# Kernel tuning notes

Measured on AMD Instinct MI355X. Metric: run time of the kernel, lower is better.

## Reference

```python
import jax, jax.numpy as jnp
import numpy as np

N, T, D, H, E, ED = 4096, 16, 5, 128, 32768, 32

def _leaky(x):
    return jnp.where(x >= 0, x, 0.2 * x)

def _lstm(x, Wih, Whh, bih, bhh):
    # x: [N, T, D] -> hidden sequence [N, T, H]; PyTorch gate order i,f,g,o
    pre = jnp.einsum('ntd,gd->tng', x, Wih) + bih + bhh  # [T, N, 4H]
    Hd = Whh.shape[1]
    def step(carry, p):
        h, c = carry
        g = p + h @ Whh.T
        i, f, gg, o = jnp.split(g, 4, axis=-1)
        c = jax.nn.sigmoid(f) * c + jax.nn.sigmoid(i) * jnp.tanh(gg)
        h = jax.nn.sigmoid(o) * jnp.tanh(c)
        return (h, c), h
    z = jnp.zeros((x.shape[0], Hd), x.dtype)
    _, hs = jax.lax.scan(step, (z, z), pre)
    return jnp.swapaxes(hs, 0, 1)

def _sire(x, src, dst, efeat, Wq, bq, Wk, bk, We, be, Wr, br):
    # SIREConv with agg_type='sum': m = LeakyReLU(eq[dst]+ek[src]+e); sum over in-edges; then linear_relation
    eq = x @ Wq.T + bq            # [N, T, H]
    ek = x @ Wk.T + bk            # [N, T, H]
    e = efeat @ We.T + be         # [E, H]
    m = _leaky(eq[dst] + ek[src] + e[:, None, :])  # [E, T, H]
    ft = jax.ops.segment_sum(m, dst, num_segments=x.shape[0])  # [N, T, H]
    return ft @ Wr.T + br

def _forward(stock_features, srcs, dsts, efeats, sire_ps, lstm_p, attn_p, mlp_p):
    sf = stock_features / jnp.mean(stock_features, axis=1, keepdims=True)
    sr = _lstm(sf, *lstm_p)  # [N, T, H]
    outs = [sr]
    for s, d, ef, p in zip(srcs, dsts, efeats, sire_ps):
        outs.append(_sire(sr, s, d, ef, *p))
    cat = jnp.concatenate(outs, axis=-1)  # [N, T, 4H]
    aw = jax.nn.softmax(cat @ attn_p[0].T + attn_p[1], axis=-2)  # softmax over time
    pooled = jnp.sum(cat * aw, axis=-2)   # [N, 4H]
    W1, b1, W2, b2 = mlp_p
    h = _leaky(pooled @ W1.T + b1)
    out = _leaky(h @ W2.T + b2)           # [N, 1]
    return out / sf[:, -1, 0:1] - 1.0


def setup_inputs() -> dict:
    key = jax.random.key(0)
    ks = iter(jax.random.split(key, 64))
    def nrm(shape, s=0.05):
        return jax.random.normal(next(ks), shape, jnp.float32) * s
    inp = {}
    inp['stock_features'] = jax.random.uniform(next(ks), (N, T, D), jnp.float32) + 0.5
    for g in ['wiki', 'industry', 'corr']:
        inp[g + '_src'] = jax.random.randint(next(ks), (E,), 0, N, jnp.int32)
        inp[g + '_dst'] = jax.random.randint(next(ks), (E,), 0, N, jnp.int32)
        inp[g + '_efeat'] = nrm((E, ED), 1.0)
        inp[g + '_Wq'] = nrm((H, H)); inp[g + '_bq'] = nrm((H,))
        inp[g + '_Wk'] = nrm((H, H)); inp[g + '_bk'] = nrm((H,))
        inp[g + '_We'] = nrm((H, ED)); inp[g + '_be'] = nrm((H,))
        inp[g + '_Wr'] = nrm((H, H)); inp[g + '_br'] = nrm((H,))
    inp['lstm_Wih'] = nrm((4 * H, D)); inp['lstm_Whh'] = nrm((4 * H, H))
    inp['lstm_bih'] = nrm((4 * H,)); inp['lstm_bhh'] = nrm((4 * H,))
    inp['attn_W'] = nrm((1, 4 * H)); inp['attn_b'] = nrm((1,))
    inp['mlp_W1'] = nrm((H, 4 * H)); inp['mlp_b1'] = nrm((H,))
    inp['mlp_W2'] = nrm((1, H)); inp['mlp_b2'] = nrm((1,))
    return inp


def reference(stock_features, wiki_src, wiki_dst, wiki_efeat,
              wiki_Wq, wiki_bq, wiki_Wk, wiki_bk, wiki_We, wiki_be, wiki_Wr, wiki_br,
              industry_src, industry_dst, industry_efeat,
              industry_Wq, industry_bq, industry_Wk, industry_bk, industry_We, industry_be, industry_Wr, industry_br,
              corr_src, corr_dst, corr_efeat,
              corr_Wq, corr_bq, corr_Wk, corr_bk, corr_We, corr_be, corr_Wr, corr_br,
              lstm_Wih, lstm_Whh, lstm_bih, lstm_bhh,
              attn_W, attn_b, mlp_W1, mlp_b1, mlp_W2, mlp_b2):
    srcs = (wiki_src, industry_src, corr_src)
    dsts = (wiki_dst, industry_dst, corr_dst)
    efeats = (wiki_efeat, industry_efeat, corr_efeat)
    sire_ps = ((wiki_Wq, wiki_bq, wiki_Wk, wiki_bk, wiki_We, wiki_be, wiki_Wr, wiki_br),
               (industry_Wq, industry_bq, industry_Wk, industry_bk, industry_We, industry_be, industry_Wr, industry_br),
               (corr_Wq, corr_bq, corr_Wk, corr_bk, corr_We, corr_be, corr_Wr, corr_br))
    return _forward(stock_features, srcs, dsts, efeats, sire_ps,
                    (lstm_Wih, lstm_Whh, lstm_bih, lstm_bhh),
                    (attn_W, attn_b), (mlp_W1, mlp_b1, mlp_W2, mlp_b2))
```

## Files before the change

kernel.cpp:

```cpp
#include <hip/hip_runtime.h>
#include <cstdint>
#include <cstddef>

#define NS 4096
#define TS 16
#define DF 5
#define HD 128
#define EE 32768
#define EDD 32

typedef _Float16 h16;
typedef __attribute__((ext_vector_type(8))) _Float16 f16x8;
typedef __attribute__((ext_vector_type(2))) __fp16 fp16x2_n;
typedef __attribute__((ext_vector_type(4))) float f32x4;

__device__ __forceinline__ float sigmoidf_(float x){ return 1.f/(1.f+__expf(-x)); }
__device__ __forceinline__ float tanhf_(float x){ return 1.f - 2.f/(1.f+__expf(2.f*x)); }
__device__ __forceinline__ float leaky_(float x){ return x >= 0.f ? x : 0.2f*x; }

__device__ __forceinline__ unsigned pkh(float a, float b){
  union { fp16x2_n h; unsigned u; } x;
  x.h = __builtin_amdgcn_cvt_pkrtz(a, b);
  return x.u;
}
__device__ __forceinline__ void unpkh(unsigned u, float& a, float& b){
  union { unsigned u; fp16x2_n h; } x; x.u = u;
  a = (float)x.h.x; b = (float)x.h.y;
}
__device__ __forceinline__ f16x8 ld_h8(const h16* p){
  union { uint4 u; f16x8 v; } x; x.u = *(const uint4*)p; return x.v;
}

template<int AH, int CH>
__device__ __forceinline__ void gemm_dev(const void* Av, int lda,
    const float* __restrict__ Bp, int ldb, const float* __restrict__ bp,
    void* Cv, int ldc, int K, int act, size_t m0,
    h16* Asb, h16* Bsb)
{
  int tid = threadIdx.x;
  int wv = tid>>6, lane = tid&63, lm = lane&15, lq = lane>>4;
  f32x4 acc[2][8];
  #pragma unroll
  for (int mt=0;mt<2;mt++)
    #pragma unroll
    for (int nt=0;nt<8;nt++)
      acc[mt][nt] = (f32x4){0.f,0.f,0.f,0.f};

  for (int k0=0; k0<K; k0+=32){
    if (AH){
      const h16* A = (const h16*)Av;
      #pragma unroll
      for (int rep=0;rep<2;rep++){
        int idx = tid + rep*256;
        int row = idx>>2, c8 = idx&3;
        *(uint4*)&Asb[row*40 + c8*8] = *(const uint4*)&A[(m0+row)*(size_t)lda + k0 + c8*8];
      }
    } else {
      const float* A = (const float*)Av;
      #pragma unroll
      for (int rep=0;rep<4;rep++){
        int idx = tid + rep*256;
        int row = idx>>3, c4 = idx&7;
        float4 a = *(const float4*)&A[(m0+row)*(size_t)lda + k0 + c4*4];
        *(uint2*)&Asb[row*40 + c4*4] = make_uint2(pkh(a.x,a.y), pkh(a.z,a.w));
      }
    }
    #pragma unroll
    for (int rep=0;rep<4;rep++){
      int idx = tid + rep*256;
      int row = idx>>3, c4 = idx&7;
      float4 b = *(const float4*)&Bp[(size_t)row*ldb + k0 + c4*4];
      *(uint2*)&Bsb[row*40 + c4*4] = make_uint2(pkh(b.x,b.y), pkh(b.z,b.w));
    }
    __syncthreads();
    f16x8 afr[2], bfr[8];
    #pragma unroll
    for (int mt=0;mt<2;mt++)
      afr[mt] = ld_h8(&Asb[(wv*32 + mt*16 + lm)*40 + lq*8]);
    #pragma unroll
    for (int nt=0;nt<8;nt++)
      bfr[nt] = ld_h8(&Bsb[(nt*16 + lm)*40 + lq*8]);
    #pragma unroll
    for (int mt=0;mt<2;mt++)
      #pragma unroll
      for (int nt=0;nt<8;nt++)
        acc[mt][nt] = __builtin_amdgcn_mfma_f32_16x16x32_f16(afr[mt], bfr[nt], acc[mt][nt], 0,0,0);
    __syncthreads();
  }

  #pragma unroll
  for (int mt=0;mt<2;mt++){
    #pragma unroll
    for (int nt=0;nt<8;nt++){
      int col = nt*16 + lm;
      float bv = bp[col];
      #pragma unroll
      for (int i=0;i<4;i++){
        float o = acc[mt][nt][i] + bv;
        if (act) o = leaky_(o);
        size_t ridx = (m0 + wv*32 + mt*16 + lq*4 + i)*(size_t)ldc + col;
        if (CH) ((h16*)Cv)[ridx] = (h16)o;
        else    ((float*)Cv)[ridx] = o;
      }
    }
  }
}

__device__ void lstm8_dev(int blk, const float* __restrict__ sf,
                          const h16* __restrict__ WhhH,
                          const float* __restrict__ Wih, const float* __restrict__ bih,
                          const float* __restrict__ bhh, h16* __restrict__ cat,
                          char* smem)
{
  float* gates = (float*)smem;
  h16* hbuf = (h16*)(smem+16512);
  float* sfb = (float*)(smem+16512+2176);
  int tid = threadIdx.x;
  int n0 = blk*8;
  int wv = tid>>6, lane = tid&63, lm = lane&15, lq = lane>>4;

  f16x8 bfr[8][4];
  #pragma unroll
  for (int nt=0;nt<8;nt++){
    int g = wv*128 + nt*16 + lm;
    #pragma unroll
    for (int kt=0;kt<4;kt++)
      bfr[nt][kt] = *(const f16x8*)&WhhH[g*128 + kt*32 + lq*8];
  }

  int j = tid & 127;
  int rb = tid >> 7;
  float wih[4][5]; float bsum[4];
  #pragma unroll
  for (int gi=0; gi<4; gi++){
    int gc = gi*128 + j;
    #pragma unroll
    for (int d=0; d<5; d++) wih[gi][d] = Wih[gc*5+d];
    bsum[gi] = bih[gc] + bhh[gc];
  }
  float cst[4] = {0.f,0.f,0.f,0.f};

  for (int i=tid;i<544;i+=256) ((unsigned*)hbuf)[i] = 0;
  for (int i=tid;i<640;i+=256) sfb[i] = sf[(size_t)n0*80 + i];
  __syncthreads();

  f16x8 zf = {0,0,0,0,0,0,0,0};
  for (int t=0;t<16;t++){
    f16x8 af[4];
    #pragma unroll
    for (int kt=0;kt<4;kt++)
      af[kt] = (lm < 8) ? *(const f16x8*)&hbuf[lm*136 + kt*32 + lq*8] : zf;
    #pragma unroll
    for (int nt=0;nt<8;nt++){
      f32x4 acc = {0.f,0.f,0.f,0.f};
      #pragma unroll
      for (int kt=0;kt<4;kt++)
        acc = __builtin_amdgcn_mfma_f32_16x16x32_f16(af[kt], bfr[nt][kt], acc, 0,0,0);
      if (lq < 2){
        int col = wv*128 + nt*16 + lm;
        #pragma unroll
        for (int i=0;i<4;i++)
          gates[(lq*4+i)*516 + col] = acc[i];
      }
    }
    __syncthreads();
    #pragma unroll
    for (int q=0;q<4;q++){
      int r = rb + 2*q;
      const float* s = &sfb[r*80 + t*5];
      float pre[4];
      #pragma unroll
      for (int gi=0;gi<4;gi++){
        float a = bsum[gi];
        #pragma unroll
        for (int d=0;d<5;d++) a = fmaf(s[d], wih[gi][d], a);
        pre[gi] = a + gates[r*516 + gi*128 + j];
      }
      float iv = sigmoidf_(pre[0]);
      float fv = sigmoidf_(pre[1]);
      float gv = tanhf_(pre[2]);
      float ov = sigmoidf_(pre[3]);
      float c = fv*cst[q] + iv*gv;
      cst[q] = c;
      float h = ov*tanhf_(c);
      h16 hh = (h16)h;
      hbuf[r*136 + j] = hh;
      cat[(size_t)((n0+r)*16 + t)*512 + j] = hh;
    }
    __syncthreads();
  }
}

struct PP { const float* Wr[3]; };
__global__ __launch_bounds__(256)
void k_prolog(const float* __restrict__ x, float* __restrict__ sf,
              const float* __restrict__ Whh, h16* __restrict__ whhH,
              int* __restrict__ cnt, PP wr, h16* __restrict__ wrH)
{
  int b = blockIdx.x, tid = threadIdx.x;
  if (b < 48){
    int i = b*256 + tid;
    if (i < 3*4096) cnt[i] = 0;
  } else if (b < 128){
    int id = (b-48)*256 + tid;
    if (id < NS*DF){
      int n = id / DF, d = id % DF;
      const float* xp = x + (size_t)n*TS*DF + d;
      float s = 0.f;
      #pragma unroll
      for (int t=0;t<TS;t++) s += xp[t*DF];
      float inv = (float)TS / s;
      float* sp = sf + (size_t)n*TS*DF + d;
      #pragma unroll
      for (int t=0;t<TS;t++) sp[t*DF] = xp[t*DF]*inv;
    }
  } else if (b < 384){
    int i = (b-128)*256 + tid;
    whhH[i] = (h16)Whh[i];
  } else {
    int i = (b-384)*256 + tid;
    int g = i >> 14, r = i & 16383;
    wrH[i] = (h16)wr.Wr[g][r];
  }
}

struct M1 {
  const float *sf, *Wih, *bih, *bhh;
  const h16* WhhH;
  h16* cat;
  const float *ef[3]; const float *We[3]; const float *be[3];
  h16* eeb;
  const int* dst[3]; const int* src[3];
  int* cnt;
  int2* eidx2;
};
__global__ __launch_bounds__(256,2)
void k_mega1(M1 p)
{
  __shared__ __align__(16) char smem[21504];
  int b = blockIdx.x;
  if (b < 512){
    lstm8_dev(b, p.sf, p.WhhH, p.Wih, p.bih, p.bhh, p.cat, smem);
  } else if (b < 1280){
    int idx = b - 512;
    int proj = idx % 3, mt = idx / 3;
    h16* Asb = (h16*)smem;
    h16* Bsb = Asb + 128*40;
    gemm_dev<0,1>(p.ef[proj], 32, p.We[proj], 32, p.be[proj],
                  p.eeb + (size_t)proj*EE*128, 128, 32, 0, (size_t)mt*128, Asb, Bsb);
  } else {
    int idx = b - 1280;
    int g = idx >> 7, blk = idx & 127;
    int e = blk*256 + threadIdx.x;
    int d = p.dst[g][e];
    int s = p.src[g][e];
    int pos = atomicAdd(&p.cnt[g*4096 + d], 1);
    if (pos < 32) p.eidx2[((size_t)(g*4096 + d))*32 + pos] = make_int2(e, s);
  }
}

struct M2 {
  const h16* cat;
  const float* W[6]; const float* bias[6];
  h16* eqk;
};
__global__ __launch_bounds__(256)
void k_mega2(M2 p)
{
  __shared__ __align__(16) h16 Asb[128*40];
  __shared__ __align__(16) h16 Bsb[128*40];
  int b = blockIdx.x;
  int proj = b % 6, mt = b / 6;
  gemm_dev<1,1>(p.cat, 512, p.W[proj], 128, p.bias[proj],
                p.eqk + (size_t)proj*NS*TS*128, 128, 128, 0, (size_t)mt*128, Asb, Bsb);
}

struct EWP { const float* br[3]; };
__global__ __launch_bounds__(256)
void k_edgewr(const h16* __restrict__ eqk, const h16* __restrict__ eeb,
              const int* __restrict__ cnt, const int2* __restrict__ eidx2,
              const h16* __restrict__ wrH, EWP wp, h16* __restrict__ cat)
{
  __shared__ __align__(16) h16 ftS[16*136];
  int n = blockIdx.x;
  int g = blockIdx.y;
  const h16* eqb = eqk + (size_t)(2*g)  *NS*TS*128;
  const h16* ekb = eqk + (size_t)(2*g+1)*NS*TS*128;
  const h16* eeg = eeb + (size_t)g*EE*128;
  int tid = threadIdx.x;
  int wv = tid>>6, lane = tid&63, lm = lane&15, lq = lane>>4;

  const h16* wrg = wrH + (size_t)g*128*128;
  f16x8 bfr[2][4];
  #pragma unroll
  for (int nn=0;nn<2;nn++){
    int row = (wv*2+nn)*16 + lm;
    #pragma unroll
    for (int kt=0;kt<4;kt++)
      bfr[nn][kt] = ld_h8(&wrg[row*128 + kt*32 + lq*8]);
  }

  int t = tid>>4, hb = (tid&15)*8;
  size_t own = ((size_t)(n*16+t))*128 + hb;
  f16x8 eqv = ld_h8(&eqb[own]);
  const f16x8 c02 = {(h16)0.2f,(h16)0.2f,(h16)0.2f,(h16)0.2f,
                     (h16)0.2f,(h16)0.2f,(h16)0.2f,(h16)0.2f};
  float acc[8];
  #pragma unroll
  for (int j=0;j<8;j++) acc[j]=0.f;
  int ne = cnt[g*4096 + n]; if (ne > 32) ne = 32;
  const int2* el = eidx2 + ((size_t)(g*4096 + n))*32;
  for (int i=0;i<ne;i++){
    int2 es = el[i];
    f16x8 kv = ld_h8(&ekb[((size_t)(es.y*16+t))*128 + hb]);
    f16x8 ev = ld_h8(&eeg[(size_t)es.x*128 + hb]);
    f16x8 x = eqv + kv + ev;
    f16x8 lk = __builtin_elementwise_max(x, x*c02);
    #pragma unroll
    for (int j=0;j<8;j++) acc[j] += (float)lk[j];
  }
  uint4 o;
  o.x = pkh(acc[0],acc[1]); o.y = pkh(acc[2],acc[3]);
  o.z = pkh(acc[4],acc[5]); o.w = pkh(acc[6],acc[7]);
  *(uint4*)&ftS[t*136 + hb] = o;
  __syncthreads();

  f16x8 af[4];
  #pragma unroll
  for (int kt=0;kt<4;kt++)
    af[kt] = ld_h8(&ftS[lm*136 + kt*32 + lq*8]);
  const float* br = wp.br[g];
  h16* catp = cat + (size_t)(1+g)*128;
  #pragma unroll
  for (int nn=0; nn<2; nn++){
    int nt = wv*2 + nn;
    f32x4 a2 = {0.f,0.f,0.f,0.f};
    #pragma unroll
    for (int kt=0;kt<4;kt++)
      a2 = __builtin_amdgcn_mfma_f32_16x16x32_f16(af[kt], bfr[nn][kt], a2, 0,0,0);
    int colg = nt*16 + lm;
    float bv = br[colg];
    #pragma unroll
    for (int i=0;i<4;i++){
      int row = lq*4 + i;
      catp[((size_t)(n*16+row))*512 + colg] = (h16)(a2[i] + bv);
    }
  }
}

__global__ __launch_bounds__(256)
void k_attn(const h16* __restrict__ cat, const float* __restrict__ attnW,
            const float* __restrict__ attnB, h16* __restrict__ pooled)
{
  __shared__ h16 ct[16*512];
  __shared__ float sred[4][16];
  int n = blockIdx.x, tid = threadIdx.x;
  {
    const uint4* srcp = (const uint4*)(cat + (size_t)n*8192);
    uint4* dstp = (uint4*)ct;
    for (int i=tid;i<1024;i+=256) dstp[i] = srcp[i];
  }
  __syncthreads();
  int c0 = tid*2;
  float w0 = attnW[c0], w1 = attnW[c0+1];
  const unsigned* ctu = (const unsigned*)ct;
  float loc[16];
  #pragma unroll
  for (int t=0;t<16;t++){
    float a,b; unpkh(ctu[t*256 + tid], a, b);
    loc[t] = a*w0 + b*w1;
  }
  #pragma unroll
  for (int t=0;t<16;t++){
    float v = loc[t];
    for (int off=1; off<64; off<<=1) v += __shfl_xor(v, off, 64);
    loc[t]=v;
  }
  int wave = tid >> 6, lane = tid & 63;
  if (lane==0){
    #pragma unroll
    for (int t=0;t<16;t++) sred[wave][t]=loc[t];
  }
  __syncthreads();
  float s[16]; float m=-1e30f;
  float ab = attnB[0];
  #pragma unroll
  for (int t=0;t<16;t++){ s[t] = sred[0][t]+sred[1][t]+sred[2][t]+sred[3][t] + ab; m = fmaxf(m, s[t]); }
  float sum=0.f;
  #pragma unroll
  for (int t=0;t<16;t++){ s[t] = __expf(s[t]-m); sum += s[t]; }
  float inv = 1.f/sum;
  float p0=0.f,p1=0.f;
  #pragma unroll
  for (int t=0;t<16;t++){
    float a = s[t]*inv;
    float x,y; unpkh(ctu[t*256 + tid], x, y);
    p0 = fmaf(x, a, p0); p1 = fmaf(y, a, p1);
  }
  ((unsigned*)pooled)[(size_t)n*256 + tid] = pkh(p0,p1);
}

__global__ __launch_bounds__(256)
void k_mlp(const h16* __restrict__ pooled, const float* __restrict__ W1,
           const float* __restrict__ b1, h16* __restrict__ hmlp,
           const float* __restrict__ W2, const float* __restrict__ b2,
           const float* __restrict__ sf, float* __restrict__ out)
{
  __shared__ __align__(16) h16 Asb[128*40];
  __shared__ __align__(16) h16 Bsb[128*40];
  size_t m0 = (size_t)blockIdx.x*128;
  gemm_dev<1,1>(pooled, 512, W1, 512, b1, hmlp, 128, 512, 1, m0, Asb, Bsb);
  __syncthreads();
  int tid = threadIdx.x;
  int r = tid >> 1, o64 = (tid & 1)*64;
  const h16* hp = hmlp + (m0 + r)*128 + o64;
  float acc = 0.f;
  #pragma unroll
  for (int c=0; c<64; c++) acc = fmaf((float)hp[c], W2[o64 + c], acc);
  acc += __shfl_xor(acc, 1, 64);
  if ((tid & 1) == 0){
    float o = leaky_(acc + b2[0]);
    size_t n = m0 + r;
    out[n] = o / sf[n*80 + 75] - 1.f;
  }
}

extern "C" void kernel_launch(void* const* d_in, const int* in_sizes, int n_in,
                              void* d_out, int out_size, void* d_ws, size_t ws_size,
                              hipStream_t stream)
{
  const float* x    = (const float*)d_in[0];
  const float* Wih  = (const float*)d_in[34];
  const float* Whh  = (const float*)d_in[35];
  const float* bih  = (const float*)d_in[36];
  const float* bhh  = (const float*)d_in[37];
  const float* attnW= (const float*)d_in[38];
  const float* attnB= (const float*)d_in[39];
  const float* W1   = (const float*)d_in[40];
  const float* b1   = (const float*)d_in[41];
  const float* W2   = (const float*)d_in[42];
  const float* b2   = (const float*)d_in[43];

  char* w = (char*)d_ws;
  size_t o = 0;
  h16* cat    = (h16*)(w+o); o += (size_t)NS*TS*512*2;
  h16* eqk    = (h16*)(w+o); o += (size_t)6*NS*TS*128*2;
  h16* eeb    = (h16*)(w+o); o += (size_t)3*EE*128*2;
  h16* pooled = (h16*)(w+o); o += (size_t)NS*512*2;
  float* sf   = (float*)(w+o); o += (size_t)NS*TS*DF*4;
  h16* hmlp   = (h16*)(w+o); o += (size_t)NS*HD*2;
  h16* whhH   = (h16*)(w+o); o += (size_t)512*128*2;
  h16* wrH    = (h16*)(w+o); o += (size_t)3*128*128*2;
  int* cnt    = (int*)(w+o); o += 3*4096*4;
  int2* eidx2 = (int2*)(w+o); o += (size_t)3*4096*32*8;

  {
    PP pp;
    for (int g=0; g<3; g++) pp.Wr[g] = (const float*)d_in[1 + g*11 + 9];
    k_prolog<<<576, 256, 0, stream>>>(x, sf, Whh, whhH, cnt, pp, wrH);
  }

  {
    M1 p;
    p.sf = sf; p.Wih = Wih; p.bih = bih; p.bhh = bhh;
    p.WhhH = whhH; p.cat = cat; p.eeb = eeb; p.cnt = cnt; p.eidx2 = eidx2;
    for (int g=0; g<3; g++){
      int base = 1 + g*11;
      p.src[g] = (const int*)d_in[base+0];
      p.dst[g] = (const int*)d_in[base+1];
      p.ef[g] = (const float*)d_in[base+2];
      p.We[g] = (const float*)d_in[base+7];
      p.be[g] = (const float*)d_in[base+8];
    }
    k_mega1<<<1664, 256, 0, stream>>>(p);
  }

  {
    M2 p;
    p.cat = cat; p.eqk = eqk;
    for (int g=0; g<3; g++){
      int base = 1 + g*11;
      p.W[2*g]      = (const float*)d_in[base+3];
      p.bias[2*g]   = (const float*)d_in[base+4];
      p.W[2*g+1]    = (const float*)d_in[base+5];
      p.bias[2*g+1] = (const float*)d_in[base+6];
    }
    k_mega2<<<3072, 256, 0, stream>>>(p);
  }

  {
    EWP wp;
    for (int g=0; g<3; g++) wp.br[g] = (const float*)d_in[1 + g*11 + 10];
    k_edgewr<<<dim3(NS,3), 256, 0, stream>>>(eqk, eeb, cnt, eidx2, wrH, wp, cat);
  }

  k_attn<<<NS, 256, 0, stream>>>(cat, attnW, attnB, pooled);
  k_mlp<<<32, 256, 0, stream>>>(pooled, W1, b1, hmlp, W2, b2, sf, (float*)d_out);
}
```

Measured before the change: 365.6 us.

## Fuse query projection into edge aggregation kernel, drop eq buffer

The per-node query projection (eq = sr @ Wq^T + bq) moves out of the batched projection GEMM and into the edge aggregation kernel. Each block now computes its node's 16x128 eq tile with MFMA from the LSTM output in shared memory. This halves the projection GEMM launch and removes the write and re-read of three eq tensors in global memory. In exchange, Wq is converted to fp16 in the prolog, and the Wq/Wr B-fragments are loaded inside the MFMA loops rather than preloaded, which adds extra shared memory and syncs to the edge kernel.

```diff
diff --git a/kernel.cpp b/kernel.cpp
--- a/kernel.cpp
+++ b/kernel.cpp
@@ -191,11 +191,12 @@
   }
 }
 
-struct PP { const float* Wr[3]; };
+struct PP { const float* Wr[3]; const float* Wq[3]; };
 __global__ __launch_bounds__(256)
 void k_prolog(const float* __restrict__ x, float* __restrict__ sf,
               const float* __restrict__ Whh, h16* __restrict__ whhH,
-              int* __restrict__ cnt, PP wr, h16* __restrict__ wrH)
+              int* __restrict__ cnt, PP wr, h16* __restrict__ wrH,
+              h16* __restrict__ wqH)
 {
   int b = blockIdx.x, tid = threadIdx.x;
   if (b < 48){
@@ -217,10 +218,14 @@
   } else if (b < 384){
     int i = (b-128)*256 + tid;
     whhH[i] = (h16)Whh[i];
-  } else {
+  } else if (b < 576){
     int i = (b-384)*256 + tid;
     int g = i >> 14, r = i & 16383;
     wrH[i] = (h16)wr.Wr[g][r];
+  } else {
+    int i = (b-576)*256 + tid;
+    int g = i >> 14, r = i & 16383;
+    wqH[i] = (h16)wr.Wq[g][r];
   }
 }
 
@@ -261,48 +266,68 @@
 
 struct M2 {
   const h16* cat;
-  const float* W[6]; const float* bias[6];
-  h16* eqk;
+  const float* Wk[3]; const float* bk[3];
+  h16* ekb;
 };
 __global__ __launch_bounds__(256)
 void k_mega2(M2 p)
 {
   __shared__ __align__(16) h16 Asb[128*40];
   __shared__ __align__(16) h16 Bsb[128*40];
-  int b = blockIdx.x;
-  int proj = b % 6, mt = b / 6;
-  gemm_dev<1,1>(p.cat, 512, p.W[proj], 128, p.bias[proj],
-                p.eqk + (size_t)proj*NS*TS*128, 128, 128, 0, (size_t)mt*128, Asb, Bsb);
-}
-
-struct EWP { const float* br[3]; };
+  int proj = blockIdx.x;
+  size_t m0 = (size_t)blockIdx.y * 128;
+  gemm_dev<1,1>(p.cat, 512, p.Wk[proj], 128, p.bk[proj],
+                p.ekb + (size_t)proj*NS*TS*128, 128, 128, 0, m0, Asb, Bsb);
+}
+
+struct EWP { const float* bq[3]; const float* br[3]; };
 __global__ __launch_bounds__(256)
-void k_edgewr(const h16* __restrict__ eqk, const h16* __restrict__ eeb,
+void k_edgewr(const h16* __restrict__ ekb, const h16* __restrict__ eeb,
               const int* __restrict__ cnt, const int2* __restrict__ eidx2,
-              const h16* __restrict__ wrH, EWP wp, h16* __restrict__ cat)
-{
+              const h16* __restrict__ wqH, const h16* __restrict__ wrH,
+              EWP wp, h16* __restrict__ cat)
+{
+  __shared__ __align__(16) h16 srS[16*136];
+  __shared__ __align__(16) h16 eqS[16*136];
   __shared__ __align__(16) h16 ftS[16*136];
   int n = blockIdx.x;
   int g = blockIdx.y;
-  const h16* eqb = eqk + (size_t)(2*g)  *NS*TS*128;
-  const h16* ekb = eqk + (size_t)(2*g+1)*NS*TS*128;
+  const h16* ekg = ekb + (size_t)g*NS*TS*128;
   const h16* eeg = eeb + (size_t)g*EE*128;
   int tid = threadIdx.x;
   int wv = tid>>6, lane = tid&63, lm = lane&15, lq = lane>>4;
-
-  const h16* wrg = wrH + (size_t)g*128*128;
-  f16x8 bfr[2][4];
-  #pragma unroll
-  for (int nn=0;nn<2;nn++){
-    int row = (wv*2+nn)*16 + lm;
+  int t = tid>>4, hb = (tid&15)*8;
+
+  *(uint4*)&srS[t*136 + hb] =
+      *(const uint4*)&cat[((size_t)(n*16+t))*512 + hb];
+  __syncthreads();
+
+  {
+    f16x8 af[4];
     #pragma unroll
     for (int kt=0;kt<4;kt++)
-      bfr[nn][kt] = ld_h8(&wrg[row*128 + kt*32 + lq*8]);
-  }
-
-  int t = tid>>4, hb = (tid&15)*8;
-  size_t own = ((size_t)(n*16+t))*128 + hb;
-  f16x8 eqv = ld_h8(&eqb[own]);
+      af[kt] = ld_h8(&srS[lm*136 + kt*32 + lq*8]);
+    const h16* wqg = wqH + (size_t)g*128*128;
+    const float* bq = wp.bq[g];
+    #pragma unroll
+    for (int nn=0; nn<2; nn++){
+      int nt = wv*2 + nn;
+      f32x4 a2 = {0.f,0.f,0.f,0.f};
+      #pragma unroll
+      for (int kt=0;kt<4;kt++){
+        f16x8 bf = ld_h8(&wqg[(nt*16+lm)*128 + kt*32 + lq*8]);
+        a2 = __builtin_amdgcn_mfma_f32_16x16x32_f16(af[kt], bf, a2, 0,0,0);
+      }
+      int colg = nt*16 + lm;
+      float bv = bq[colg];
+      #pragma unroll
+      for (int i=0;i<4;i++)
+        eqS[(lq*4+i)*136 + colg] = (h16)(a2[i] + bv);
+    }
+  }
+  __syncthreads();
+
+  f16x8 eqv = ld_h8(&eqS[t*136 + hb]);
   const f16x8 c02 = {(h16)0.2f,(h16)0.2f,(h16)0.2f,(h16)0.2f,
                      (h16)0.2f,(h16)0.2f,(h16)0.2f,(h16)0.2f};
   float acc[8];
@@ -312,7 +337,7 @@
   const int2* el = eidx2 + ((size_t)(g*4096 + n))*32;
   for (int i=0;i<ne;i++){
     int2 es = el[i];
-    f16x8 kv = ld_h8(&ekb[((size_t)(es.y*16+t))*128 + hb]);
+    f16x8 kv = ld_h8(&ekg[((size_t)(es.y*16+t))*128 + hb]);
     f16x8 ev = ld_h8(&eeg[(size_t)es.x*128 + hb]);
     f16x8 x = eqv + kv + ev;
     f16x8 lk = __builtin_elementwise_max(x, x*c02);
@@ -329,6 +354,7 @@
   #pragma unroll
   for (int kt=0;kt<4;kt++)
     af[kt] = ld_h8(&ftS[lm*136 + kt*32 + lq*8]);
+  const h16* wrg = wrH + (size_t)g*128*128;
   const float* br = wp.br[g];
   h16* catp = cat + (size_t)(1+g)*128;
   #pragma unroll
@@ -336,8 +362,10 @@
     int nt = wv*2 + nn;
     f32x4 a2 = {0.f,0.f,0.f,0.f};
     #pragma unroll
-    for (int kt=0;kt<4;kt++)
-      a2 = __builtin_amdgcn_mfma_f32_16x16x32_f16(af[kt], bfr[nn][kt], a2, 0,0,0);
+    for (int kt=0;kt<4;kt++){
+      f16x8 bf = ld_h8(&wrg[(nt*16+lm)*128 + kt*32 + lq*8]);
+      a2 = __builtin_amdgcn_mfma_f32_16x16x32_f16(af[kt], bf, a2, 0,0,0);
+    }
     int colg = nt*16 + lm;
     float bv = br[colg];
     #pragma unroll
@@ -444,20 +472,24 @@
   char* w = (char*)d_ws;
   size_t o = 0;
   h16* cat    = (h16*)(w+o); o += (size_t)NS*TS*512*2;
-  h16* eqk    = (h16*)(w+o); o += (size_t)6*NS*TS*128*2;
+  h16* ekb    = (h16*)(w+o); o += (size_t)3*NS*TS*128*2;
   h16* eeb    = (h16*)(w+o); o += (size_t)3*EE*128*2;
   h16* pooled = (h16*)(w+o); o += (size_t)NS*512*2;
   float* sf   = (float*)(w+o); o += (size_t)NS*TS*DF*4;
   h16* hmlp   = (h16*)(w+o); o += (size_t)NS*HD*2;
   h16* whhH   = (h16*)(w+o); o += (size_t)512*128*2;
   h16* wrH    = (h16*)(w+o); o += (size_t)3*128*128*2;
+  h16* wqH    = (h16*)(w+o); o += (size_t)3*128*128*2;
   int* cnt    = (int*)(w+o); o += 3*4096*4;
   int2* eidx2 = (int2*)(w+o); o += (size_t)3*4096*32*8;
 
   {
     PP pp;
-    for (int g=0; g<3; g++) pp.Wr[g] = (const float*)d_in[1 + g*11 + 9];
-    k_prolog<<<576, 256, 0, stream>>>(x, sf, Whh, whhH, cnt, pp, wrH);
+    for (int g=0; g<3; g++){
+      pp.Wr[g] = (const float*)d_in[1 + g*11 + 9];
+      pp.Wq[g] = (const float*)d_in[1 + g*11 + 3];
+    }
+    k_prolog<<<768, 256, 0, stream>>>(x, sf, Whh, whhH, cnt, pp, wrH, wqH);
   }
 
   {
@@ -477,21 +509,22 @@
 
   {
     M2 p;
-    p.cat = cat; p.eqk = eqk;
+    p.cat = cat; p.ekb = ekb;
     for (int g=0; g<3; g++){
       int base = 1 + g*11;
-      p.W[2*g]      = (const float*)d_in[base+3];
-      p.bias[2*g]   = (const float*)d_in[base+4];
-      p.W[2*g+1]    = (const float*)d_in[base+5];
-      p.bias[2*g+1] = (const float*)d_in[base+6];
-    }
-    k_mega2<<<3072, 256, 0, stream>>>(p);
+      p.Wk[g] = (const float*)d_in[base+5];
+      p.bk[g] = (const float*)d_in[base+6];
+    }
+    k_mega2<<<dim3(3,512), 256, 0, stream>>>(p);
   }
 
   {
     EWP wp;
-    for (int g=0; g<3; g++) wp.br[g] = (const float*)d_in[1 + g*11 + 10];
-    k_edgewr<<<dim3(NS,3), 256, 0, stream>>>(eqk, eeb, cnt, eidx2, wrH, wp, cat);
+    for (int g=0; g<3; g++){
+      wp.bq[g] = (const float*)d_in[1 + g*11 + 4];
+      wp.br[g] = (const float*)d_in[1 + g*11 + 10];
+    }
+    k_edgewr<<<dim3(NS,3), 256, 0, stream>>>(ekb, eeb, cnt, eidx2, wqH, wrH, wp, cat);
   }
 
   k_attn<<<NS, 256, 0, stream>>>(cat, attnW, attnB, pooled);
```

Result: slower. 392.1 us (+7.2%).

## Fuse edge aggregation, relation linear and attention pooling into one kernel

Applied to the files above, without the earlier changes.

The per-graph edge aggregation kernel and the attention-pooling kernel become a single per-node kernel that loops over the three graphs and keeps the whole [16,512] concatenated tile in shared memory. The global cat buffer shrinks to an LSTM-only [N,T,128] output, so the full concatenated tensor is never written to or read back from global memory and one launch goes away. In exchange each block does the three graphs serially (fewer blocks, NS instead of NS×3) and reloads Wr fragments per MFMA instead of holding them in registers.

```diff
diff --git a/kernel.cpp b/kernel.cpp
--- a/kernel.cpp
+++ b/kernel.cpp
@@ -109,7 +109,7 @@
 __device__ void lstm8_dev(int blk, const float* __restrict__ sf,
                           const h16* __restrict__ WhhH,
                           const float* __restrict__ Wih, const float* __restrict__ bih,
-                          const float* __restrict__ bhh, h16* __restrict__ cat,
+                          const float* __restrict__ bhh, h16* __restrict__ srG,
                           char* smem)
 {
   float* gates = (float*)smem;
@@ -185,7 +185,7 @@
       float h = ov*tanhf_(c);
       h16 hh = (h16)h;
       hbuf[r*136 + j] = hh;
-      cat[(size_t)((n0+r)*16 + t)*512 + j] = hh;
+      srG[(size_t)((n0+r)*16 + t)*128 + j] = hh;
     }
     __syncthreads();
   }
@@ -227,7 +227,7 @@
 struct M1 {
   const float *sf, *Wih, *bih, *bhh;
   const h16* WhhH;
-  h16* cat;
+  h16* srG;
   const float *ef[3]; const float *We[3]; const float *be[3];
   h16* eeb;
   const int* dst[3]; const int* src[3];
@@ -240,7 +240,7 @@
   __shared__ __align__(16) char smem[21504];
   int b = blockIdx.x;
   if (b < 512){
-    lstm8_dev(b, p.sf, p.WhhH, p.Wih, p.bih, p.bhh, p.cat, smem);
+    lstm8_dev(b, p.sf, p.WhhH, p.Wih, p.bih, p.bhh, p.srG, smem);
   } else if (b < 1280){
     int idx = b - 512;
     int proj = idx % 3, mt = idx / 3;
@@ -260,7 +260,7 @@
 }
 
 struct M2 {
-  const h16* cat;
+  const h16* srG;
   const float* W[6]; const float* bias[6];
   h16* eqk;
 };
@@ -271,130 +271,115 @@
   __shared__ __align__(16) h16 Bsb[128*40];
   int b = blockIdx.x;
   int proj = b % 6, mt = b / 6;
-  gemm_dev<1,1>(p.cat, 512, p.W[proj], 128, p.bias[proj],
+  gemm_dev<1,1>(p.srG, 128, p.W[proj], 128, p.bias[proj],
                 p.eqk + (size_t)proj*NS*TS*128, 128, 128, 0, (size_t)mt*128, Asb, Bsb);
 }
 
 struct EWP { const float* br[3]; };
 __global__ __launch_bounds__(256)
-void k_edgewr(const h16* __restrict__ eqk, const h16* __restrict__ eeb,
-              const int* __restrict__ cnt, const int2* __restrict__ eidx2,
-              const h16* __restrict__ wrH, EWP wp, h16* __restrict__ cat)
-{
+void k_edgeattn(const h16* __restrict__ srG, const h16* __restrict__ eqk,
+                const h16* __restrict__ eeb, const int* __restrict__ cnt,
+                const int2* __restrict__ eidx2, const h16* __restrict__ wrH,
+                EWP wp, const float* __restrict__ attnW,
+                const float* __restrict__ attnB, h16* __restrict__ pooled)
+{
+  __shared__ __align__(16) h16 ctS[16*520];
   __shared__ __align__(16) h16 ftS[16*136];
+  __shared__ float sred[4][16];
   int n = blockIdx.x;
-  int g = blockIdx.y;
-  const h16* eqb = eqk + (size_t)(2*g)  *NS*TS*128;
-  const h16* ekb = eqk + (size_t)(2*g+1)*NS*TS*128;
-  const h16* eeg = eeb + (size_t)g*EE*128;
   int tid = threadIdx.x;
   int wv = tid>>6, lane = tid&63, lm = lane&15, lq = lane>>4;
-
-  const h16* wrg = wrH + (size_t)g*128*128;
-  f16x8 bfr[2][4];
-  #pragma unroll
-  for (int nn=0;nn<2;nn++){
-    int row = (wv*2+nn)*16 + lm;
-    #pragma unroll
-    for (int kt=0;kt<4;kt++)
-      bfr[nn][kt] = ld_h8(&wrg[row*128 + kt*32 + lq*8]);
-  }
-
   int t = tid>>4, hb = (tid&15)*8;
-  size_t own = ((size_t)(n*16+t))*128 + hb;
-  f16x8 eqv = ld_h8(&eqb[own]);
+
+  *(uint4*)&ctS[t*520 + hb] = *(const uint4*)&srG[((size_t)(n*16+t))*128 + hb];
+
   const f16x8 c02 = {(h16)0.2f,(h16)0.2f,(h16)0.2f,(h16)0.2f,
                      (h16)0.2f,(h16)0.2f,(h16)0.2f,(h16)0.2f};
-  float acc[8];
-  #pragma unroll
-  for (int j=0;j<8;j++) acc[j]=0.f;
-  int ne = cnt[g*4096 + n]; if (ne > 32) ne = 32;
-  const int2* el = eidx2 + ((size_t)(g*4096 + n))*32;
-  for (int i=0;i<ne;i++){
-    int2 es = el[i];
-    f16x8 kv = ld_h8(&ekb[((size_t)(es.y*16+t))*128 + hb]);
-    f16x8 ev = ld_h8(&eeg[(size_t)es.x*128 + hb]);
-    f16x8 x = eqv + kv + ev;
-    f16x8 lk = __builtin_elementwise_max(x, x*c02);
-    #pragma unroll
-    for (int j=0;j<8;j++) acc[j] += (float)lk[j];
-  }
-  uint4 o;
-  o.x = pkh(acc[0],acc[1]); o.y = pkh(acc[2],acc[3]);
-  o.z = pkh(acc[4],acc[5]); o.w = pkh(acc[6],acc[7]);
-  *(uint4*)&ftS[t*136 + hb] = o;
-  __syncthreads();
-
-  f16x8 af[4];
-  #pragma unroll
-  for (int kt=0;kt<4;kt++)
-    af[kt] = ld_h8(&ftS[lm*136 + kt*32 + lq*8]);
-  const float* br = wp.br[g];
-  h16* catp = cat + (size_t)(1+g)*128;
-  #pragma unroll
-  for (int nn=0; nn<2; nn++){
-    int nt = wv*2 + nn;
-    f32x4 a2 = {0.f,0.f,0.f,0.f};
+
+  for (int g=0; g<3; g++){
+    const h16* eqb = eqk + (size_t)(2*g)  *NS*TS*128;
+    const h16* ekb = eqk + (size_t)(2*g+1)*NS*TS*128;
+    const h16* eeg = eeb + (size_t)g*EE*128;
+
+    size_t own = ((size_t)(n*16+t))*128 + hb;
+    f16x8 eqv = ld_h8(&eqb[own]);
+    float acc[8];
+    #pragma unroll
+    for (int j=0;j<8;j++) acc[j]=0.f;
+    int ne = cnt[g*4096 + n]; if (ne > 32) ne = 32;
+    const int2* el = eidx2 + ((size_t)(g*4096 + n))*32;
+    for (int i=0;i<ne;i++){
+      int2 es = el[i];
+      f16x8 kv = ld_h8(&ekb[((size_t)(es.y*16+t))*128 + hb]);
+      f16x8 ev = ld_h8(&eeg[(size_t)es.x*128 + hb]);
+      f16x8 x = eqv + kv + ev;
+      f16x8 lk = __builtin_elementwise_max(x, x*c02);
+      #pragma unroll
+      for (int j=0;j<8;j++) acc[j] += (float)lk[j];
+    }
+    uint4 o;
+    o.x = pkh(acc[0],acc[1]); o.y = pkh(acc[2],acc[3]);
+    o.z = pkh(acc[4],acc[5]); o.w = pkh(acc[6],acc[7]);
+    *(uint4*)&ftS[t*136 + hb] = o;
+    __syncthreads();
+
+    f16x8 af[4];
     #pragma unroll
     for (int kt=0;kt<4;kt++)
-      a2 = __builtin_amdgcn_mfma_f32_16x16x32_f16(af[kt], bfr[nn][kt], a2, 0,0,0);
-    int colg = nt*16 + lm;
-    float bv = br[colg];
-    #pragma unroll
-    for (int i=0;i<4;i++){
-      int row = lq*4 + i;
-      catp[((size_t)(n*16+row))*512 + colg] = (h16)(a2[i] + bv);
-    }
-  }
-}
-
-__global__ __launch_bounds__(256)
-void k_attn(const h16* __restrict__ cat, const float* __restrict__ attnW,
-            const float* __restrict__ attnB, h16* __restrict__ pooled)
-{
-  __shared__ h16 ct[16*512];
-  __shared__ float sred[4][16];
-  int n = blockIdx.x, tid = threadIdx.x;
-  {
-    const uint4* srcp = (const uint4*)(cat + (size_t)n*8192);
-    uint4* dstp = (uint4*)ct;
-    for (int i=tid;i<1024;i+=256) dstp[i] = srcp[i];
-  }
-  __syncthreads();
+      af[kt] = ld_h8(&ftS[lm*136 + kt*32 + lq*8]);
+    const h16* wrg = wrH + (size_t)g*128*128;
+    const float* br = wp.br[g];
+    #pragma unroll
+    for (int nn=0; nn<2; nn++){
+      int nt = wv*2 + nn;
+      f32x4 a2 = {0.f,0.f,0.f,0.f};
+      #pragma unroll
+      for (int kt=0;kt<4;kt++){
+        f16x8 bf = ld_h8(&wrg[(nt*16+lm)*128 + kt*32 + lq*8]);
+        a2 = __builtin_amdgcn_mfma_f32_16x16x32_f16(af[kt], bf, a2, 0,0,0);
+      }
+      int colg = (1+g)*128 + nt*16 + lm;
+      float bv = br[nt*16 + lm];
+      #pragma unroll
+      for (int i=0;i<4;i++)
+        ctS[(lq*4+i)*520 + colg] = (h16)(a2[i] + bv);
+    }
+    __syncthreads();
+  }
+
   int c0 = tid*2;
   float w0 = attnW[c0], w1 = attnW[c0+1];
-  const unsigned* ctu = (const unsigned*)ct;
+  const unsigned* ctu = (const unsigned*)ctS;
   float loc[16];
   #pragma unroll
-  for (int t=0;t<16;t++){
-    float a,b; unpkh(ctu[t*256 + tid], a, b);
-    loc[t] = a*w0 + b*w1;
-  }
-  #pragma unroll
-  for (int t=0;t<16;t++){
-    float v = loc[t];
+  for (int tt=0;tt<16;tt++){
+    float a,b; unpkh(ctu[tt*260 + tid], a, b);
+    loc[tt] = a*w0 + b*w1;
+  }
+  #pragma unroll
+  for (int tt=0;tt<16;tt++){
+    float v = loc[tt];
     for (int off=1; off<64; off<<=1) v += __shfl_xor(v, off, 64);
-    loc[t]=v;
-  }
-  int wave = tid >> 6, lane = tid & 63;
+    loc[tt]=v;
+  }
   if (lane==0){
     #pragma unroll
-    for (int t=0;t<16;t++) sred[wave][t]=loc[t];
+    for (int tt=0;tt<16;tt++) sred[wv][tt]=loc[tt];
   }
   __syncthreads();
   float s[16]; float m=-1e30f;
   float ab = attnB[0];
   #pragma unroll
-  for (int t=0;t<16;t++){ s[t] = sred[0][t]+sred[1][t]+sred[2][t]+sred[3][t] + ab; m = fmaxf(m, s[t]); }
+  for (int tt=0;tt<16;tt++){ s[tt] = sred[0][tt]+sred[1][tt]+sred[2][tt]+sred[3][tt] + ab; m = fmaxf(m, s[tt]); }
   float sum=0.f;
   #pragma unroll
-  for (int t=0;t<16;t++){ s[t] = __expf(s[t]-m); sum += s[t]; }
+  for (int tt=0;tt<16;tt++){ s[tt] = __expf(s[tt]-m); sum += s[tt]; }
   float inv = 1.f/sum;
   float p0=0.f,p1=0.f;
   #pragma unroll
-  for (int t=0;t<16;t++){
-    float a = s[t]*inv;
-    float x,y; unpkh(ctu[t*256 + tid], x, y);
+  for (int tt=0;tt<16;tt++){
+    float a = s[tt]*inv;
+    float x,y; unpkh(ctu[tt*260 + tid], x, y);
     p0 = fmaf(x, a, p0); p1 = fmaf(y, a, p1);
   }
   ((unsigned*)pooled)[(size_t)n*256 + tid] = pkh(p0,p1);
@@ -443,7 +428,7 @@
 
   char* w = (char*)d_ws;
   size_t o = 0;
-  h16* cat    = (h16*)(w+o); o += (size_t)NS*TS*512*2;
+  h16* srG    = (h16*)(w+o); o += (size_t)NS*TS*128*2;
   h16* eqk    = (h16*)(w+o); o += (size_t)6*NS*TS*128*2;
   h16* eeb    = (h16*)(w+o); o += (size_t)3*EE*128*2;
   h16* pooled = (h16*)(w+o); o += (size_t)NS*512*2;
@@ -463,7 +448,7 @@
   {
     M1 p;
     p.sf = sf; p.Wih = Wih; p.bih = bih; p.bhh = bhh;
-    p.WhhH = whhH; p.cat = cat; p.eeb = eeb; p.cnt = cnt; p.eidx2 = eidx2;
+    p.WhhH = whhH; p.srG = srG; p.eeb = eeb; p.cnt = cnt; p.eidx2 = eidx2;
     for (int g=0; g<3; g++){
       int base = 1 + g*11;
       p.src[g] = (const int*)d_in[base+0];
@@ -477,7 +462,7 @@
 
   {
     M2 p;
-    p.cat = cat; p.eqk = eqk;
+    p.srG = srG; p.eqk = eqk;
     for (int g=0; g<3; g++){
       int base = 1 + g*11;
       p.W[2*g]      = (const float*)d_in[base+3];
@@ -491,9 +476,9 @@
   {
     EWP wp;
     for (int g=0; g<3; g++) wp.br[g] = (const float*)d_in[1 + g*11 + 10];
-    k_edgewr<<<dim3(NS,3), 256, 0, stream>>>(eqk, eeb, cnt, eidx2, wrH, wp, cat);
-  }
-
-  k_attn<<<NS, 256, 0, stream>>>(cat, attnW, attnB, pooled);
+    k_edgeattn<<<NS, 256, 0, stream>>>(srG, eqk, eeb, cnt, eidx2, wrH, wp,
+                                       attnW, attnB, pooled);
+  }
+
   k_mlp<<<32, 256, 0, stream>>>(pooled, W1, b1, hmlp, W2, b2, sf, (float*)d_out);
 }
```

Result: faster. 349.5 us (median of 2 runs) (-4.4%).
